# Kernel optimization log

Hardware: AMD Instinct MI355X
Metric: run time of the kernel (lower is better)

The kernel has to match this reference:

```python
import jax, jax.numpy as jnp
import numpy as np

TEMPERATURE = 0.1
EPS = 1e-12  # matches torch F.normalize default eps


def setup_inputs() -> dict:
    key = jax.random.key(0)
    k1, k2 = jax.random.split(key)
    B, D = 4096, 512
    features1 = jax.random.normal(k1, (B, D), dtype=jnp.float32)
    features2 = jax.random.normal(k2, (B, D), dtype=jnp.float32)
    return {"features1": features1, "features2": features2}


def _l2_normalize(x, axis=1):
    norm = jnp.linalg.norm(x, axis=axis, keepdims=True)
    return x / jnp.maximum(norm, EPS)


def reference(features1, features2):
    B = features1.shape[0]
    f1 = _l2_normalize(features1)
    f2 = _l2_normalize(features2)
    features = jnp.concatenate([f1, f2], axis=0)  # (2B, D)
    sim = jnp.matmul(features, features.T) / TEMPERATURE  # (2B, 2B)
    # mask self-similarity on the diagonal with -inf
    diag = jnp.eye(2 * B, dtype=bool)
    sim = jnp.where(diag, -jnp.inf, sim)
    # positive pair labels: row i pairs with i+B (first half) / i-B (second half)
    labels = jnp.concatenate([jnp.arange(B) + B, jnp.arange(B)], axis=0)
    log_probs = jax.nn.log_softmax(sim, axis=-1)  # (2B, 2B)
    nll = -jnp.take_along_axis(log_probs, labels[:, None], axis=1)[:, 0]
    return jnp.mean(nll)
```

## Files before the change

kernel.cpp:

```cpp
#include <hip/hip_runtime.h>

#define NROWS 8192
#define HALF_N 4096
#define DIM 512
#define INV_T 10.0f
#define NRB 64
#define NBLOCKS 2080

typedef __attribute__((ext_vector_type(8))) short short8;
typedef __attribute__((ext_vector_type(4))) float f32x4;

__device__ __forceinline__ ushort f32_to_bf16_rne(float x) {
  unsigned u = __float_as_uint(x);
  unsigned r = (u + 0x7fffu + ((u >> 16) & 1u)) >> 16;
  return (ushort)r;
}

__device__ __forceinline__ void async16(const void* g, void* l) {
  __builtin_amdgcn_global_load_lds(
      (const __attribute__((address_space(1))) unsigned int*)g,
      (__attribute__((address_space(3))) unsigned int*)l, 16, 0, 0);
}

__global__ __launch_bounds__(256) void norm_cast_k(
    const float* __restrict__ f1, const float* __restrict__ f2,
    ushort* __restrict__ Fn, float* __restrict__ rowsum) {
  int wave = threadIdx.x >> 6;
  int lane = threadIdx.x & 63;
  int row = blockIdx.x * 4 + wave;
  const float* src = (row < HALF_N) ? (f1 + (size_t)row * DIM)
                                    : (f2 + (size_t)(row - HALF_N) * DIM);
  const float4* p = reinterpret_cast<const float4*>(src + lane * 8);
  float4 v0 = p[0];
  float4 v1 = p[1];
  float ss = v0.x*v0.x + v0.y*v0.y + v0.z*v0.z + v0.w*v0.w
           + v1.x*v1.x + v1.y*v1.y + v1.z*v1.z + v1.w*v1.w;
  #pragma unroll
  for (int off = 1; off < 64; off <<= 1) ss += __shfl_xor(ss, off);
  float scale = 1.0f / fmaxf(sqrtf(ss), 1e-12f);
  union { ushort u[8]; short8 v; } o;
  o.u[0] = f32_to_bf16_rne(v0.x * scale);
  o.u[1] = f32_to_bf16_rne(v0.y * scale);
  o.u[2] = f32_to_bf16_rne(v0.z * scale);
  o.u[3] = f32_to_bf16_rne(v0.w * scale);
  o.u[4] = f32_to_bf16_rne(v1.x * scale);
  o.u[5] = f32_to_bf16_rne(v1.y * scale);
  o.u[6] = f32_to_bf16_rne(v1.z * scale);
  o.u[7] = f32_to_bf16_rne(v1.w * scale);
  *reinterpret_cast<short8*>(Fn + (size_t)row * DIM + lane * 8) = o.v;
  if (lane == 0) rowsum[row] = 0.0f;
}

__global__ __launch_bounds__(256, 3) void sym_gemm_k(
    const ushort* __restrict__ Fn, float* __restrict__ rowsum,
    float* __restrict__ pairsim) {
  int bx = blockIdx.x;
  int gbx = (bx & 7) * (NBLOCKS / 8) + (bx >> 3);
  int rb = 0, rem = gbx;
  while (rem >= NRB - rb) { rem -= NRB - rb; ++rb; }
  const int cb = rb + rem;
  const int row0 = rb * 128, col0 = cb * 128;

  const int tid = threadIdx.x;
  const int wave = tid >> 6;
  const int lane = tid & 63;
  const int quad = lane >> 4;
  const int colid = lane & 15;
  const int wr0 = (wave >> 1) * 64;
  const int wc0 = (wave & 1) * 64;

  __shared__ ushort Alds[128 * 32];
  __shared__ ushort Blds[128 * 32];
  __shared__ float redrow[128];
  __shared__ float redcol[128];

  if (tid < 128) { redrow[tid] = 0.0f; redcol[tid] = 0.0f; }

  const char* FnB = (const char*)Fn;
  const char* srcA[2]; const char* srcB[2];
  ushort* dstA[2]; ushort* dstB[2];
  #pragma unroll
  for (int seg = 0; seg < 2; ++seg) {
    int inst = wave + seg * 4;
    int r = inst * 16 + (lane >> 2);
    int c = (lane & 3) ^ ((r >> 1) & 3);
    srcA[seg] = FnB + (size_t)(row0 + r) * (DIM * 2) + c * 16;
    srcB[seg] = FnB + (size_t)(col0 + r) * (DIM * 2) + c * 16;
    dstA[seg] = Alds + inst * 512;
    dstB[seg] = Blds + inst * 512;
  }

  const ushort* afp[4]; const ushort* bfp[4];
  #pragma unroll
  for (int t = 0; t < 4; ++t) {
    int r = wr0 + t * 16 + colid;
    afp[t] = Alds + r * 32 + (quad ^ ((r >> 1) & 3)) * 8;
    int c = wc0 + t * 16 + colid;
    bfp[t] = Blds + c * 32 + (quad ^ ((c >> 1) & 3)) * 8;
  }

  f32x4 acc[4][4];
  #pragma unroll
  for (int t = 0; t < 4; ++t)
    #pragma unroll
    for (int u = 0; u < 4; ++u) acc[t][u] = (f32x4){0.f, 0.f, 0.f, 0.f};

  for (int kc = 0; kc < 16; ++kc) {
    __syncthreads();
    const int koff = kc * 64;
    #pragma unroll
    for (int seg = 0; seg < 2; ++seg) {
      async16(srcA[seg] + koff, dstA[seg]);
      async16(srcB[seg] + koff, dstB[seg]);
    }
    __syncthreads();

    short8 af[4], bf[4];
    #pragma unroll
    for (int t = 0; t < 4; ++t) af[t] = *reinterpret_cast<const short8*>(afp[t]);
    #pragma unroll
    for (int t = 0; t < 4; ++t) bf[t] = *reinterpret_cast<const short8*>(bfp[t]);
    #pragma unroll
    for (int t = 0; t < 4; ++t)
      #pragma unroll
      for (int u = 0; u < 4; ++u)
        acc[t][u] = __builtin_amdgcn_mfma_f32_16x16x32_bf16(af[t], bf[u], acc[t][u], 0, 0, 0);
  }

  float re[4][4];
  float ce[4];
  #pragma unroll
  for (int t = 0; t < 4; ++t)
    #pragma unroll
    for (int r = 0; r < 4; ++r) re[t][r] = 0.0f;
  #pragma unroll
  for (int u = 0; u < 4; ++u) ce[u] = 0.0f;

  #pragma unroll
  for (int t = 0; t < 4; ++t) {
    #pragma unroll
    for (int u = 0; u < 4; ++u) {
      f32x4 a = acc[t][u];
      const int gc = col0 + wc0 + u * 16 + colid;
      #pragma unroll
      for (int r = 0; r < 4; ++r) {
        int grow = row0 + wr0 + t * 16 + quad * 4 + r;
        float sim = a[r] * INV_T;
        float e = (gc > grow) ? __expf(sim) : 0.0f;
        re[t][r] += e;
        ce[u] += e;
        if (gc == grow + HALF_N && grow < HALF_N) {
          pairsim[grow] = sim;
          pairsim[gc] = sim;
        }
      }
    }
  }

  #pragma unroll
  for (int t = 0; t < 4; ++t)
    #pragma unroll
    for (int r = 0; r < 4; ++r) {
      float v = re[t][r];
      v += __shfl_xor(v, 1); v += __shfl_xor(v, 2);
      v += __shfl_xor(v, 4); v += __shfl_xor(v, 8);
      if (colid == 0) atomicAdd(&redrow[wr0 + t * 16 + quad * 4 + r], v);
    }
  #pragma unroll
  for (int u = 0; u < 4; ++u) {
    float v = ce[u];
    v += __shfl_xor(v, 16); v += __shfl_xor(v, 32);
    if (lane < 16) atomicAdd(&redcol[wc0 + u * 16 + colid], v);
  }
  __syncthreads();
  if (tid < 128) atomicAdd(&rowsum[row0 + tid], redrow[tid]);
  else           atomicAdd(&rowsum[col0 + tid - 128], redcol[tid - 128]);
}

__global__ __launch_bounds__(1024) void finalize_k(
    const float* __restrict__ rowsum, const float* __restrict__ pairsim,
    float* __restrict__ out) {
  float local = 0.0f;
  for (int i = threadIdx.x; i < NROWS; i += 1024)
    local += logf(rowsum[i]) - pairsim[i];
  #pragma unroll
  for (int off = 1; off < 64; off <<= 1) local += __shfl_xor(local, off);
  __shared__ float red[16];
  int wave = threadIdx.x >> 6;
  int lane = threadIdx.x & 63;
  if (lane == 0) red[wave] = local;
  __syncthreads();
  if (threadIdx.x == 0) {
    float s = 0.0f;
    #pragma unroll
    for (int w = 0; w < 16; ++w) s += red[w];
    out[0] = s * (1.0f / (float)NROWS);
  }
}

extern "C" void kernel_launch(void* const* d_in, const int* in_sizes, int n_in,
                              void* d_out, int out_size, void* d_ws, size_t ws_size,
                              hipStream_t stream) {
  const float* f1 = (const float*)d_in[0];
  const float* f2 = (const float*)d_in[1];
  ushort* Fn = (ushort*)d_ws;
  float* rowsum = (float*)((char*)d_ws + (size_t)NROWS * DIM * 2);
  float* pairsim = rowsum + NROWS;
  float* out = (float*)d_out;

  norm_cast_k<<<NROWS / 4, 256, 0, stream>>>(f1, f2, Fn, rowsum);
  sym_gemm_k<<<NBLOCKS, 256, 0, stream>>>(Fn, rowsum, pairsim);
  finalize_k<<<1, 1024, 0, stream>>>(rowsum, pairsim, out);
}
```

Before: 126.9 us.

## Double K-tile depth to 64 and fuse finalize into GEMM via last-block counter

Raises the K chunk per LDS stage from 32 to 64 bf16 elements with a new XOR swizzle, halving the number of barrier-separated load rounds. It also removes the separate finalize kernel: each GEMM block bumps an atomic counter and the last block computes the log-sum reduction, saving a kernel launch. Pairsim stores become atomic exchanges so the last block reads coherent values. The larger LDS footprint may lower occupancy, and the single-block tail reduction runs with 256 threads instead of 1024.

```diff
diff --git a/kernel.cpp b/kernel.cpp
--- a/kernel.cpp
+++ b/kernel.cpp
@@ -6,6 +6,9 @@
 #define INV_T 10.0f
 #define NRB 64
 #define NBLOCKS 2080
+#define BK 64
+#define ROWB 128
+#define ROUNDS 8
 
 typedef __attribute__((ext_vector_type(8))) short short8;
 typedef __attribute__((ext_vector_type(4))) float f32x4;
@@ -24,7 +27,8 @@
 
 __global__ __launch_bounds__(256) void norm_cast_k(
     const float* __restrict__ f1, const float* __restrict__ f2,
-    ushort* __restrict__ Fn, float* __restrict__ rowsum) {
+    ushort* __restrict__ Fn, float* __restrict__ rowsum,
+    unsigned* __restrict__ cnt) {
   int wave = threadIdx.x >> 6;
   int lane = threadIdx.x & 63;
   int row = blockIdx.x * 4 + wave;
@@ -49,11 +53,13 @@
   o.u[7] = f32_to_bf16_rne(v1.w * scale);
   *reinterpret_cast<short8*>(Fn + (size_t)row * DIM + lane * 8) = o.v;
   if (lane == 0) rowsum[row] = 0.0f;
+  if (blockIdx.x == 0 && threadIdx.x == 0) *cnt = 0u;
 }
 
 __global__ __launch_bounds__(256, 3) void sym_gemm_k(
     const ushort* __restrict__ Fn, float* __restrict__ rowsum,
-    float* __restrict__ pairsim) {
+    float* __restrict__ pairsim, unsigned* __restrict__ cnt,
+    float* __restrict__ out) {
   int bx = blockIdx.x;
   int gbx = (bx & 7) * (NBLOCKS / 8) + (bx >> 3);
   int rb = 0, rem = gbx;
@@ -69,34 +75,35 @@
   const int wr0 = (wave >> 1) * 64;
   const int wc0 = (wave & 1) * 64;
 
-  __shared__ ushort Alds[128 * 32];
-  __shared__ ushort Blds[128 * 32];
+  __shared__ ushort Alds[128 * BK];
+  __shared__ ushort Blds[128 * BK];
   __shared__ float redrow[128];
   __shared__ float redcol[128];
+  __shared__ float fred[4];
+  __shared__ unsigned lastflag;
 
   if (tid < 128) { redrow[tid] = 0.0f; redcol[tid] = 0.0f; }
 
   const char* FnB = (const char*)Fn;
-  const char* srcA[2]; const char* srcB[2];
-  ushort* dstA[2]; ushort* dstB[2];
-  #pragma unroll
-  for (int seg = 0; seg < 2; ++seg) {
-    int inst = wave + seg * 4;
-    int r = inst * 16 + (lane >> 2);
-    int c = (lane & 3) ^ ((r >> 1) & 3);
-    srcA[seg] = FnB + (size_t)(row0 + r) * (DIM * 2) + c * 16;
-    srcB[seg] = FnB + (size_t)(col0 + r) * (DIM * 2) + c * 16;
-    dstA[seg] = Alds + inst * 512;
-    dstB[seg] = Blds + inst * 512;
-  }
-
-  const ushort* afp[4]; const ushort* bfp[4];
+  const int lrow = lane >> 3;
+  const int clog = (lane & 7) ^ lrow;
+  const size_t laneoff = (size_t)lrow * (DIM * 2) + (size_t)clog * 16;
+  const char* srcA = FnB + (size_t)(row0 + wave * 32) * (DIM * 2) + laneoff;
+  const char* srcB = FnB + (size_t)(col0 + wave * 32) * (DIM * 2) + laneoff;
+  ushort* dstA = Alds + wave * 32 * BK;
+  ushort* dstB = Blds + wave * 32 * BK;
+
+  const ushort* afp[4][2];
+  const ushort* bfp[4][2];
   #pragma unroll
   for (int t = 0; t < 4; ++t) {
-    int r = wr0 + t * 16 + colid;
-    afp[t] = Alds + r * 32 + (quad ^ ((r >> 1) & 3)) * 8;
-    int c = wc0 + t * 16 + colid;
-    bfp[t] = Blds + c * 32 + (quad ^ ((c >> 1) & 3)) * 8;
+    int ra = wr0 + t * 16 + colid;
+    int rc = wc0 + t * 16 + colid;
+    #pragma unroll
+    for (int s = 0; s < 2; ++s) {
+      afp[t][s] = Alds + ra * BK + (((s * 4 + quad) ^ (ra & 7)) << 3);
+      bfp[t][s] = Blds + rc * BK + (((s * 4 + quad) ^ (rc & 7)) << 3);
+    }
   }
 
   f32x4 acc[4][4];
@@ -105,26 +112,29 @@
     #pragma unroll
     for (int u = 0; u < 4; ++u) acc[t][u] = (f32x4){0.f, 0.f, 0.f, 0.f};
 
-  for (int kc = 0; kc < 16; ++kc) {
+  for (int kc = 0; kc < ROUNDS; ++kc) {
     __syncthreads();
-    const int koff = kc * 64;
-    #pragma unroll
-    for (int seg = 0; seg < 2; ++seg) {
-      async16(srcA[seg] + koff, dstA[seg]);
-      async16(srcB[seg] + koff, dstB[seg]);
+    const size_t ko = (size_t)kc * ROWB;
+    #pragma unroll
+    for (int j = 0; j < 4; ++j) {
+      async16(srcA + (size_t)j * 8192 + ko, dstA + j * 512);
+      async16(srcB + (size_t)j * 8192 + ko, dstB + j * 512);
     }
     __syncthreads();
 
-    short8 af[4], bf[4];
-    #pragma unroll
-    for (int t = 0; t < 4; ++t) af[t] = *reinterpret_cast<const short8*>(afp[t]);
-    #pragma unroll
-    for (int t = 0; t < 4; ++t) bf[t] = *reinterpret_cast<const short8*>(bfp[t]);
-    #pragma unroll
-    for (int t = 0; t < 4; ++t)
-      #pragma unroll
-      for (int u = 0; u < 4; ++u)
-        acc[t][u] = __builtin_amdgcn_mfma_f32_16x16x32_bf16(af[t], bf[u], acc[t][u], 0, 0, 0);
+    #pragma unroll
+    for (int s = 0; s < 2; ++s) {
+      short8 af[4], bf[4];
+      #pragma unroll
+      for (int t = 0; t < 4; ++t) af[t] = *reinterpret_cast<const short8*>(afp[t][s]);
+      #pragma unroll
+      for (int u = 0; u < 4; ++u) bf[u] = *reinterpret_cast<const short8*>(bfp[u][s]);
+      #pragma unroll
+      for (int t = 0; t < 4; ++t)
+        #pragma unroll
+        for (int u = 0; u < 4; ++u)
+          acc[t][u] = __builtin_amdgcn_mfma_f32_16x16x32_bf16(af[t], bf[u], acc[t][u], 0, 0, 0);
+    }
   }
 
   float re[4][4];
@@ -150,8 +160,8 @@
         re[t][r] += e;
         ce[u] += e;
         if (gc == grow + HALF_N && grow < HALF_N) {
-          pairsim[grow] = sim;
-          pairsim[gc] = sim;
+          atomicExch(&pairsim[grow], sim);
+          atomicExch(&pairsim[gc], sim);
         }
       }
     }
@@ -175,26 +185,24 @@
   __syncthreads();
   if (tid < 128) atomicAdd(&rowsum[row0 + tid], redrow[tid]);
   else           atomicAdd(&rowsum[col0 + tid - 128], redcol[tid - 128]);
-}
-
-__global__ __launch_bounds__(1024) void finalize_k(
-    const float* __restrict__ rowsum, const float* __restrict__ pairsim,
-    float* __restrict__ out) {
-  float local = 0.0f;
-  for (int i = threadIdx.x; i < NROWS; i += 1024)
-    local += logf(rowsum[i]) - pairsim[i];
-  #pragma unroll
-  for (int off = 1; off < 64; off <<= 1) local += __shfl_xor(local, off);
-  __shared__ float red[16];
-  int wave = threadIdx.x >> 6;
-  int lane = threadIdx.x & 63;
-  if (lane == 0) red[wave] = local;
   __syncthreads();
-  if (threadIdx.x == 0) {
-    float s = 0.0f;
-    #pragma unroll
-    for (int w = 0; w < 16; ++w) s += red[w];
-    out[0] = s * (1.0f / (float)NROWS);
+
+  if (tid == 0) {
+    __threadfence();
+    lastflag = (atomicAdd(cnt, 1u) == NBLOCKS - 1) ? 1u : 0u;
+  }
+  __syncthreads();
+  if (lastflag) {
+    __threadfence();
+    float local = 0.0f;
+    for (int i = tid; i < NROWS; i += 256)
+      local += logf(rowsum[i]) - pairsim[i];
+    #pragma unroll
+    for (int off = 1; off < 64; off <<= 1) local += __shfl_xor(local, off);
+    if (lane == 0) fred[wave] = local;
+    __syncthreads();
+    if (tid == 0)
+      out[0] = (fred[0] + fred[1] + fred[2] + fred[3]) * (1.0f / (float)NROWS);
   }
 }
 
@@ -206,9 +214,9 @@
   ushort* Fn = (ushort*)d_ws;
   float* rowsum = (float*)((char*)d_ws + (size_t)NROWS * DIM * 2);
   float* pairsim = rowsum + NROWS;
+  unsigned* cnt = (unsigned*)(pairsim + NROWS);
   float* out = (float*)d_out;
 
-  norm_cast_k<<<NROWS / 4, 256, 0, stream>>>(f1, f2, Fn, rowsum);
-  sym_gemm_k<<<NBLOCKS, 256, 0, stream>>>(Fn, rowsum, pairsim);
-  finalize_k<<<1, 1024, 0, stream>>>(rowsum, pairsim, out);
-}
+  norm_cast_k<<<NROWS / 4, 256, 0, stream>>>(f1, f2, Fn, rowsum, cnt);
+  sym_gemm_k<<<NBLOCKS, 256, 0, stream>>>(Fn, rowsum, pairsim, cnt, out);
+}
```

New measurement: 156.0 us. 23.0% more time.
